# Kernel optimization log

Measured on AMD Instinct MI355X. Metric: run time of the kernel, lower is better.

The kernel has to match this reference:

```python
import jax, jax.numpy as jnp
import numpy as np

B, L, DM, H = 2, 2048, 1024, 16
D = DM // H  # head_dim = key_dim = 64


def setup_inputs() -> dict:
    key = jax.random.key(0)
    ks = jax.random.split(key, 6)
    w = 0.02
    return {
        "x": jax.random.normal(ks[0], (B, L, DM), dtype=jnp.float32),
        "wq_attn": jax.random.normal(ks[1], (DM, H * D), dtype=jnp.float32) * w,
        "wk_attn": jax.random.normal(ks[2], (DM, H * D), dtype=jnp.float32) * w,
        "wq_rel": jax.random.normal(ks[3], (DM, H * D), dtype=jnp.float32) * w,
        "wk_rel": jax.random.normal(ks[4], (DM, H * D), dtype=jnp.float32) * w,
        "wo": jax.random.normal(ks[5], (H * D, H * D), dtype=jnp.float32) * w,
    }


def reference(x, wq_attn, wk_attn, wq_rel, wk_rel, wo):
    b, l, dm = x.shape
    # projections -> (B, L, H, D); MHA so n_kv_heads == n_heads, no repeat_kv
    q = (x @ wq_attn).reshape(b, l, H, D)
    k = (x @ wk_attn).reshape(b, l, H, D)
    qr = (x @ wq_rel).reshape(b, l, H, D)
    kr = (x @ wk_rel).reshape(b, l, H, D)

    scale = D ** -0.5  # SDPA default: 1/sqrt(query key_dim)
    scores = jnp.einsum("blhd,bmhd->bhlm", q, k) * scale  # (B, H, L, L)
    causal = jnp.tril(jnp.ones((l, l), dtype=bool))
    scores = jnp.where(causal, scores, -jnp.inf)
    attn = jax.nn.softmax(scores, axis=-1)

    # attend over relational keys, then Hadamard with relational queries
    attended_kr = jnp.einsum("bhlm,bmhd->blhd", attn, kr)  # (B, L, H, D)
    attended_relations = qr * attended_kr                    # (B, L, H, D)

    out = attended_relations.reshape(b, l, H * D) @ wo       # (B, L, d_model)
    return out
```

## Files before the change

### kernel.cpp

```cpp
#include <hip/hip_runtime.h>
#include <stdint.h>


typedef __attribute__((ext_vector_type(4))) float floatx4;
typedef __attribute__((ext_vector_type(8))) short shortx8;
typedef __attribute__((ext_vector_type(4))) short shortx4;

__device__ __forceinline__ unsigned short f2bf(float f) {
    unsigned u = __float_as_uint(f);
    u += 0x7fffu + ((u >> 16) & 1u);
    return (unsigned short)(u >> 16);
}
__device__ __forceinline__ float bf2f(unsigned short s) {
    return __uint_as_float(((unsigned)s) << 16);
}
__device__ __forceinline__ float exp2fast(float x) {
#if __has_builtin(__builtin_amdgcn_exp2f)
    return __builtin_amdgcn_exp2f(x);
#else
    return __expf(x * 0.69314718056f);
#endif
}
__device__ __forceinline__ unsigned pkbf(float e0, float e1) {
    return __builtin_amdgcn_perm(__float_as_uint(e1), __float_as_uint(e0), 0x07060302u);
}
__device__ __forceinline__ floatx4 mfma16(shortx4 a, shortx4 b, floatx4 c) {
#if __has_builtin(__builtin_amdgcn_mfma_f32_16x16x16bf16_1k)
    return __builtin_amdgcn_mfma_f32_16x16x16bf16_1k(a, b, c, 0, 0, 0);
#else
    shortx8 a8 = {a[0], a[1], a[2], a[3], 0, 0, 0, 0};
    shortx8 b8 = {b[0], b[1], b[2], b[3], 0, 0, 0, 0};
    return __builtin_amdgcn_mfma_f32_16x16x32_bf16(a8, b8, c, 0, 0, 0);
#endif
}
__device__ __forceinline__ void gll16(const void* g, void* l) {
    __builtin_amdgcn_global_load_lds(
        (const __attribute__((address_space(1))) unsigned int*)g,
        (__attribute__((address_space(3))) unsigned int*)l, 16, 0, 0);
}

__global__ void k_cvt_x(const float* __restrict__ x, unsigned short* __restrict__ xb) {
    int i = (blockIdx.x * 256 + threadIdx.x) * 4;
    float4 v = *(const float4*)(x + i);
    ushort4 o;
    o.x = f2bf(v.x); o.y = f2bf(v.y); o.z = f2bf(v.z); o.w = f2bf(v.w);
    *(ushort4*)(xb + i) = o;
}

__global__ __launch_bounds__(256) void k_cvt_w5(const float* __restrict__ wq,
                                                const float* __restrict__ wk,
                                                const float* __restrict__ wqr,
                                                const float* __restrict__ wkr,
                                                const float* __restrict__ wo,
                                                unsigned short* __restrict__ wcatT,
                                                unsigned short* __restrict__ wotT) {
    __shared__ unsigned short Tl[64 * 65];
    const int t = threadIdx.x;
    const int kt = blockIdx.x * 64, nt = blockIdx.y * 64;
    const int z = blockIdx.z;
    const float* W = (z == 0) ? wq : (z == 1) ? wk : (z == 2) ? wqr : (z == 3) ? wkr : wo;
    unsigned short* outT = (z < 4) ? (wcatT + (size_t)z * 1024 * 1024) : wotT;
    const float scale = (z == 0) ? 0.18033688f : 1.0f;
    {
        const int kl = t >> 3, nc = (t & 7) * 8;
        const float* src = W + (size_t)(kt + kl) * 1024 + nt + nc;
        float a[8], b[8];
        *(float4*)(a)     = *(const float4*)(src);
        *(float4*)(a + 4) = *(const float4*)(src + 4);
        *(float4*)(b)     = *(const float4*)(src + 32 * 1024);
        *(float4*)(b + 4) = *(const float4*)(src + 32 * 1024 + 4);
#pragma unroll
        for (int i = 0; i < 8; ++i) {
            Tl[kl * 65 + nc + i]        = f2bf(a[i] * scale);
            Tl[(kl + 32) * 65 + nc + i] = f2bf(b[i] * scale);
        }
    }
    __syncthreads();
    {
        const int n = t >> 2, kc = (t & 3) * 16;
        shortx8 o0, o1;
#pragma unroll
        for (int i = 0; i < 8; ++i) {
            o0[i] = (short)Tl[(kc + i) * 65 + n];
            o1[i] = (short)Tl[(kc + 8 + i) * 65 + n];
        }
        unsigned short* dst = outT + (size_t)(nt + n) * 1024 + kt + kc;
        *(shortx8*)(dst)     = o0;
        *(shortx8*)(dst + 8) = o1;
    }
}

__global__ __launch_bounds__(256) void k_trans(const unsigned short* __restrict__ qcat,
                                               unsigned short* __restrict__ krT) {
    __shared__ unsigned short Tl[64 * 65];
    const int t = threadIdx.x;
    const int mt = blockIdx.x * 64;
    const int bh = blockIdx.y;
    const int b = bh >> 4, h = bh & 15;
    {
        const int ml = t >> 3, dc = (t & 7) * 8;
        const unsigned short* src =
            qcat + ((size_t)b * 2048 + mt + ml) * 4096 + 3072 + h * 64 + dc;
        shortx8 v0 = *(const shortx8*)(src);
        shortx8 v1 = *(const shortx8*)(src + (size_t)32 * 4096);
#pragma unroll
        for (int i = 0; i < 8; ++i) {
            Tl[ml * 65 + dc + i]        = (unsigned short)v0[i];
            Tl[(ml + 32) * 65 + dc + i] = (unsigned short)v1[i];
        }
    }
    __syncthreads();
    {
        const int d = t >> 2, mc = (t & 3) * 16;
        shortx8 o0, o1;
#pragma unroll
        for (int i = 0; i < 8; ++i) {
            o0[i] = (short)Tl[(mc + i) * 65 + d];
            o1[i] = (short)Tl[(mc + 8 + i) * 65 + d];
        }
        unsigned short* dst = krT + ((size_t)bh * 64 + d) * 2048 + mt + mc;
        *(shortx8*)(dst)     = o0;
        *(shortx8*)(dst + 8) = o1;
    }
}

__global__ __launch_bounds__(512, 1) void k_gemm_bt256(const unsigned short* __restrict__ A,
                                                       const unsigned short* __restrict__ Bt,
                                                       unsigned short* __restrict__ C,
                                                       int N, int K) {
    __shared__ alignas(16) unsigned short As[4][256 * 32];
    __shared__ alignas(16) unsigned short Bs[4][256 * 32];
    const int t = threadIdx.x;
    const int lane = t & 63, w = t >> 6;
    const int ln = lane & 15, quad = lane >> 4;
    const int wm = w >> 2, wn = w & 3;
    const int flat = blockIdx.x;
    const int xcd = flat & 7, idx = flat >> 3;
    const int bm = ((xcd >> 1) * 4 + (idx >> 3)) * 256;
    const int bn = ((xcd & 1) * 8 + (idx & 7)) * 256;

    floatx4 acc[8][4] = {};

    const int srow = t >> 2;
    const int sc = (t & 3) ^ ((srow >> 1) & 3);
    const unsigned short* gA = A + (size_t)(bm + srow) * K + sc * 8;
    const unsigned short* gB = Bt + (size_t)(bn + srow) * K + sc * 8;
    const int w16 = w * 16;

    auto stage = [&](int kt, int buf) {
        const unsigned short* a = gA + (size_t)kt * 32;
        const unsigned short* b = gB + (size_t)kt * 32;
        gll16(a,                    &As[buf][w16 * 32]);
        gll16(a + (size_t)128 * K,  &As[buf][(128 + w16) * 32]);
        gll16(b,                    &Bs[buf][w16 * 32]);
        gll16(b + (size_t)128 * K,  &Bs[buf][(128 + w16) * 32]);
    };

    const int NT = K >> 5;
    stage(0, 0); stage(1, 1); stage(2, 2);

    const int sw = (ln >> 1) & 3;
    for (int t0 = 0; t0 < NT; ++t0) {
        asm volatile("" ::: "memory");
        __builtin_amdgcn_s_barrier();
        asm volatile("" ::: "memory");
        if (t0 + 3 < NT) {
            stage(t0 + 3, (t0 + 3) & 3);
            asm volatile("s_waitcnt vmcnt(12)" ::: "memory");
        } else if (t0 + 2 < NT) {
            asm volatile("s_waitcnt vmcnt(8)" ::: "memory");
        } else if (t0 + 1 < NT) {
            asm volatile("s_waitcnt vmcnt(4)" ::: "memory");
        } else {
            asm volatile("s_waitcnt vmcnt(0)" ::: "memory");
        }
        __builtin_amdgcn_s_barrier();
        asm volatile("" ::: "memory");
        const unsigned short* Ab = As[t0 & 3];
        const unsigned short* Bb = Bs[t0 & 3];
        shortx8 bfr[4];
#pragma unroll
        for (int j = 0; j < 4; ++j)
            bfr[j] = *(const shortx8*)(Bb + (wn * 64 + j * 16 + ln) * 32 + ((quad ^ sw) * 8));
#pragma unroll
        for (int i = 0; i < 8; ++i) {
            shortx8 af = *(const shortx8*)(Ab + (wm * 128 + i * 16 + ln) * 32 + ((quad ^ sw) * 8));
#pragma unroll
            for (int j = 0; j < 4; ++j)
                acc[i][j] = __builtin_amdgcn_mfma_f32_16x16x32_bf16(af, bfr[j], acc[i][j], 0, 0, 0);
        }
    }

#pragma unroll
    for (int i = 0; i < 8; ++i)
#pragma unroll
        for (int j = 0; j < 4; ++j)
#pragma unroll
            for (int r = 0; r < 4; ++r) {
                int row = bm + wm * 128 + i * 16 + quad * 4 + r;
                int col = bn + wn * 64 + j * 16 + ln;
                C[(size_t)row * N + col] = f2bf(acc[i][j][r]);
            }
}

__global__ __launch_bounds__(256) void k_gemm_n64(const unsigned short* __restrict__ A,
                                                  const unsigned short* __restrict__ Bt,
                                                  float* __restrict__ C,
                                                  int N, int K) {
    __shared__ alignas(16) unsigned short As[4][128 * 32];
    __shared__ alignas(16) unsigned short Bs[4][64 * 32];
    const int t = threadIdx.x;
    const int lane = t & 63, wv = t >> 6;
    const int ln = lane & 15, quad = lane >> 4;
    const int bm = blockIdx.y * 128, bn = blockIdx.x * 64;

    floatx4 acc[2][4] = {};

    const int srow = t >> 2;
    const int sc = (t & 3) ^ ((srow >> 1) & 3);
    const unsigned short* gA = A + (size_t)(bm + srow) * K + sc * 8;
    const unsigned short* gB = Bt + (size_t)(bn + srow) * K + sc * 8;

    auto stage = [&](int kt, int buf) {
        const unsigned short* a = gA + (size_t)kt * 32;
        gll16(a,                   &As[buf][wv * 512]);
        gll16(a + (size_t)64 * K,  &As[buf][2048 + wv * 512]);
        gll16(gB + (size_t)kt * 32, &Bs[buf][wv * 512]);
    };

    const int NT = K >> 5;
    stage(0, 0); stage(1, 1); stage(2, 2);

    const int sw = (ln >> 1) & 3;
    for (int t0 = 0; t0 < NT; ++t0) {
        asm volatile("" ::: "memory");
        __builtin_amdgcn_s_barrier();
        asm volatile("" ::: "memory");
        if (t0 + 3 < NT) {
            stage(t0 + 3, (t0 + 3) & 3);
            asm volatile("s_waitcnt vmcnt(9)" ::: "memory");
        } else if (t0 + 2 < NT) {
            asm volatile("s_waitcnt vmcnt(6)" ::: "memory");
        } else if (t0 + 1 < NT) {
            asm volatile("s_waitcnt vmcnt(3)" ::: "memory");
        } else {
            asm volatile("s_waitcnt vmcnt(0)" ::: "memory");
        }
        __builtin_amdgcn_s_barrier();
        asm volatile("" ::: "memory");
        const unsigned short* Ab = As[t0 & 3];
        const unsigned short* Bb = Bs[t0 & 3];
        shortx8 af[2], bfr[4];
#pragma unroll
        for (int i = 0; i < 2; ++i)
            af[i] = *(const shortx8*)(Ab + (wv * 32 + i * 16 + ln) * 32 + ((quad ^ sw) * 8));
#pragma unroll
        for (int j = 0; j < 4; ++j)
            bfr[j] = *(const shortx8*)(Bb + (j * 16 + ln) * 32 + ((quad ^ sw) * 8));
#pragma unroll
        for (int i = 0; i < 2; ++i)
#pragma unroll
            for (int j = 0; j < 4; ++j)
                acc[i][j] = __builtin_amdgcn_mfma_f32_16x16x32_bf16(af[i], bfr[j], acc[i][j], 0, 0, 0);
    }

#pragma unroll
    for (int i = 0; i < 2; ++i)
#pragma unroll
        for (int j = 0; j < 4; ++j)
#pragma unroll
            for (int r = 0; r < 4; ++r) {
                int row = bm + wv * 32 + i * 16 + quad * 4 + r;
                int col = bn + j * 16 + ln;
                C[(size_t)row * N + col] = acc[i][j][r];
            }
}

__global__ __launch_bounds__(256, 2) void k_attn(const unsigned short* __restrict__ qcat,
                                                 const unsigned short* __restrict__ krT,
                                                 unsigned short* __restrict__ ar) {
    __shared__ alignas(16) unsigned short Kl[2][64 * 64];
    __shared__ alignas(16) unsigned short Rl[2][64 * 64];
    __shared__ float Ls[4][4][16];

    const int t = threadIdx.x;
    const int lane = t & 63, w = t >> 6;
    const int ln = lane & 15, quad = lane >> 4;
    const int flat = blockIdx.x;
    const int bh = (flat & 7) * 4 + ((flat >> 3) & 3);
    const int qts = flat >> 5;
    const int qt = (qts & 1) ? 31 - (qts >> 1) : (qts >> 1);
    const int b = bh >> 4, h = bh & 15;
    const int l0 = qt * 64;
    const size_t baserow = (size_t)b * 2048;

    shortx8 aq[4][2];
#pragma unroll
    for (int qc = 0; qc < 4; ++qc) {
        const unsigned short* qp =
            qcat + (baserow + l0 + qc * 16 + ln) * 4096 + h * 64 + quad * 8;
        aq[qc][0] = *(const shortx8*)(qp);
        aq[qc][1] = *(const shortx8*)(qp + 32);
    }

    floatx4 acc_o[4][4] = {};
    float lsum[4] = {0.f, 0.f, 0.f, 0.f};

    const int srow = t >> 3;
    const int sc = (t & 7) ^ (srow & 7);
    const unsigned short* gK = qcat + (baserow + srow) * 4096 + 1024 + h * 64 + sc * 8;
    const unsigned short* gR = krT + ((size_t)bh * 64 + srow) * 2048 + sc * 8;

    auto stage = [&](int kt, int buf) {
        gll16(gK + (size_t)(kt * 64) * 4096,      &Kl[buf][w * 512]);
        gll16(gK + (size_t)(kt * 64 + 32) * 4096, &Kl[buf][2048 + w * 512]);
        gll16(gR + kt * 64,                       &Rl[buf][w * 512]);
        gll16(gR + (size_t)32 * 2048 + kt * 64,   &Rl[buf][2048 + w * 512]);
    };

    stage(0, 0);
    const int swz = ln & 7;
    const int krow = (w * 16 + ln) * 64;
    const int cmw = w * 2 + (quad >> 1);
    int cur = 0;
    for (int kt = 0; kt <= qt; ++kt, cur ^= 1) {
        __syncthreads();
        if (kt < qt) stage(kt + 1, cur ^ 1);
        const unsigned short* Kc = Kl[cur];
        const unsigned short* Rc = Rl[cur];
        const bool diag = (kt == qt);

        shortx8 kf0 = *(const shortx8*)(Kc + krow + ((quad ^ swz) * 8));
        shortx8 kf1 = *(const shortx8*)(Kc + krow + (((4 + quad) ^ swz) * 8));
        shortx4 krf[4];
#pragma unroll
        for (int jd = 0; jd < 4; ++jd)
            krf[jd] = *(const shortx4*)(Rc + (jd * 16 + ln) * 64 +
                                        ((cmw ^ swz) * 8) + (quad & 1) * 4);

        const int keyb = kt * 64 + w * 16 + quad * 4;
        shortx4 pk[4];
#pragma unroll
        for (int qc = 0; qc < 4; ++qc) {
            floatx4 z = {0.f, 0.f, 0.f, 0.f};
            z = __builtin_amdgcn_mfma_f32_16x16x32_bf16(kf0, aq[qc][0], z, 0, 0, 0);
            z = __builtin_amdgcn_mfma_f32_16x16x32_bf16(kf1, aq[qc][1], z, 0, 0, 0);
            float e0 = exp2fast(z[0]);
            float e1 = exp2fast(z[1]);
            float e2 = exp2fast(z[2]);
            float e3 = exp2fast(z[3]);
            if (diag) {
                const int q = l0 + qc * 16 + ln;
                e0 = (keyb + 0 > q) ? 0.f : e0;
                e1 = (keyb + 1 > q) ? 0.f : e1;
                e2 = (keyb + 2 > q) ? 0.f : e2;
                e3 = (keyb + 3 > q) ? 0.f : e3;
            }
            lsum[qc] += (e0 + e1) + (e2 + e3);
            struct U2 { unsigned a, b; } u{pkbf(e0, e1), pkbf(e2, e3)};
            pk[qc] = __builtin_bit_cast(shortx4, u);
        }

#pragma unroll
        for (int qc = 0; qc < 4; ++qc)
#pragma unroll
            for (int jd = 0; jd < 4; ++jd)
                acc_o[qc][jd] = mfma16(krf[jd], pk[qc], acc_o[qc][jd]);
    }

#pragma unroll
    for (int qc = 0; qc < 4; ++qc) {
        float s = lsum[qc];
        s += __shfl_xor(s, 16);
        s += __shfl_xor(s, 32);
        lsum[qc] = s;
    }
    if (lane < 16) {
#pragma unroll
        for (int qc = 0; qc < 4; ++qc) Ls[w][qc][lane] = lsum[qc];
    }

    __syncthreads();
    float* redA = (float*)&Kl[0][0];
    float* redB = (float*)&Rl[0][0];
    if (w >= 2) {
        float* dst = (w == 2) ? redA : redB;
#pragma unroll
        for (int qc = 0; qc < 4; ++qc)
#pragma unroll
            for (int jd = 0; jd < 4; ++jd)
                *(floatx4*)(dst + ((qc * 4 + jd) * 64 + lane) * 4) = acc_o[qc][jd];
    }
    __syncthreads();
    if (w < 2) {
        const float* src = (w == 0) ? redA : redB;
#pragma unroll
        for (int qc = 0; qc < 4; ++qc)
#pragma unroll
            for (int jd = 0; jd < 4; ++jd)
                acc_o[qc][jd] += *(const floatx4*)(src + ((qc * 4 + jd) * 64 + lane) * 4);
    }
    __syncthreads();
    if (w == 1) {
#pragma unroll
        for (int qc = 0; qc < 4; ++qc)
#pragma unroll
            for (int jd = 0; jd < 4; ++jd)
                *(floatx4*)(redA + ((qc * 4 + jd) * 64 + lane) * 4) = acc_o[qc][jd];
    }
    __syncthreads();
    if (w == 0) {
        float inv[4];
#pragma unroll
        for (int qc = 0; qc < 4; ++qc)
            inv[qc] = 1.0f / (Ls[0][qc][ln] + Ls[1][qc][ln] + Ls[2][qc][ln] + Ls[3][qc][ln]);
#pragma unroll
        for (int qc = 0; qc < 4; ++qc) {
            const int q = l0 + qc * 16 + ln;
            const unsigned short* qr = qcat + (baserow + q) * 4096 + 2048 + h * 64;
            unsigned short* arow = ar + (baserow + q) * 1024 + h * 64;
#pragma unroll
            for (int jd = 0; jd < 4; ++jd) {
                floatx4 a = acc_o[qc][jd];
                a += *(const floatx4*)(redA + ((qc * 4 + jd) * 64 + lane) * 4);
                const int d0 = jd * 16 + quad * 4;
                shortx4 qv = *(const shortx4*)(qr + d0);
                shortx4 o;
#pragma unroll
                for (int r = 0; r < 4; ++r)
                    o[r] = (short)f2bf(a[r] * inv[qc] * bf2f((unsigned short)qv[r]));
                *(shortx4*)(arow + d0) = o;
            }
        }
    }
}

extern "C" void kernel_launch(void* const* d_in, const int* in_sizes, int n_in,
                              void* d_out, int out_size, void* d_ws, size_t ws_size,
                              hipStream_t stream) {
    const float* x   = (const float*)d_in[0];
    const float* wq  = (const float*)d_in[1];
    const float* wk  = (const float*)d_in[2];
    const float* wqr = (const float*)d_in[3];
    const float* wkr = (const float*)d_in[4];
    const float* wo  = (const float*)d_in[5];
    float* out = (float*)d_out;

    unsigned short* xb    = (unsigned short*)d_ws;
    unsigned short* wcatT = xb + (size_t)4096 * 1024;
    unsigned short* qcat  = wcatT + (size_t)4096 * 1024;
    unsigned short* wotT  = qcat + (size_t)4096 * 4096;
    unsigned short* krT   = wcatT;
    unsigned short* arb   = xb;

    k_cvt_x<<<4096, 256, 0, stream>>>(x, xb);
    k_cvt_w5<<<dim3(16, 16, 5), 256, 0, stream>>>(wq, wk, wqr, wkr, wo, wcatT, wotT);
    k_gemm_bt256<<<256, 512, 0, stream>>>(xb, wcatT, qcat, 4096, 1024);
    k_trans<<<dim3(32, 32), 256, 0, stream>>>(qcat, krT);
    k_attn<<<1024, 256, 0, stream>>>(qcat, krT, arb);
    k_gemm_n64<<<dim3(16, 32), 256, 0, stream>>>(arb, wotT, out, 1024, 1024);
}
```

Measured before the change: 201.0 us.

## Interleave LDS reads, staging and MFMA phases in GEMMs; add setprio

The large projection GEMM is restructured so each K-step runs in two half-phases. Each half reads its A/B fragments from LDS, issues the global-to-LDS prefetch for A or B separately, then runs its MFMA block at raised wave priority. The goal is to overlap LDS traffic and global staging with matrix math. The N=64 output GEMM drops from a 4-stage to a simpler 2-buffer loop, relying on __syncthreads between steps, which cuts LDS use but shortens prefetch depth. The attention PV MFMA block is also wrapped in s_setprio, and the extra barriers per step add synchronisation cost.

```diff
diff --git a/kernel.cpp b/kernel.cpp
--- a/kernel.cpp
+++ b/kernel.cpp
@@ -147,48 +147,70 @@
     const unsigned short* gB = Bt + (size_t)(bn + srow) * K + sc * 8;
     const int w16 = w * 16;
 
-    auto stage = [&](int kt, int buf) {
+    auto stageA = [&](int kt, int buf) {
         const unsigned short* a = gA + (size_t)kt * 32;
+        gll16(a,                   &As[buf][w16 * 32]);
+        gll16(a + (size_t)128 * K, &As[buf][(128 + w16) * 32]);
+    };
+    auto stageB = [&](int kt, int buf) {
         const unsigned short* b = gB + (size_t)kt * 32;
-        gll16(a,                    &As[buf][w16 * 32]);
-        gll16(a + (size_t)128 * K,  &As[buf][(128 + w16) * 32]);
-        gll16(b,                    &Bs[buf][w16 * 32]);
-        gll16(b + (size_t)128 * K,  &Bs[buf][(128 + w16) * 32]);
+        gll16(b,                   &Bs[buf][w16 * 32]);
+        gll16(b + (size_t)128 * K, &Bs[buf][(128 + w16) * 32]);
     };
 
     const int NT = K >> 5;
-    stage(0, 0); stage(1, 1); stage(2, 2);
+    stageA(0, 0); stageB(0, 0);
+    stageA(1, 1); stageB(1, 1);
+    stageA(2, 2); stageB(2, 2);
+    asm volatile("s_waitcnt vmcnt(8)" ::: "memory");
+    __builtin_amdgcn_s_barrier();
 
     const int sw = (ln >> 1) & 3;
     for (int t0 = 0; t0 < NT; ++t0) {
+        const unsigned short* Ab = As[t0 & 3];
+        const unsigned short* Bb = Bs[t0 & 3];
+        const int nb = (t0 + 3) & 3;
+        shortx8 bfr0 = *(const shortx8*)(Bb + (wn * 64 + 0 * 16 + ln) * 32 + ((quad ^ sw) * 8));
+        shortx8 bfr1 = *(const shortx8*)(Bb + (wn * 64 + 1 * 16 + ln) * 32 + ((quad ^ sw) * 8));
+        shortx8 af[8];
+#pragma unroll
+        for (int i = 0; i < 8; ++i)
+            af[i] = *(const shortx8*)(Ab + (wm * 128 + i * 16 + ln) * 32 + ((quad ^ sw) * 8));
+        if (t0 + 3 < NT) stageA(t0 + 3, nb);
         asm volatile("" ::: "memory");
         __builtin_amdgcn_s_barrier();
+        asm volatile("s_waitcnt lgkmcnt(0)" ::: "memory");
+        __builtin_amdgcn_s_setprio(1);
+#pragma unroll
+        for (int i = 0; i < 8; ++i) {
+            acc[i][0] = __builtin_amdgcn_mfma_f32_16x16x32_bf16(af[i], bfr0, acc[i][0], 0, 0, 0);
+            acc[i][1] = __builtin_amdgcn_mfma_f32_16x16x32_bf16(af[i], bfr1, acc[i][1], 0, 0, 0);
+        }
+        __builtin_amdgcn_s_setprio(0);
         asm volatile("" ::: "memory");
+        __builtin_amdgcn_s_barrier();
+        shortx8 bfr2 = *(const shortx8*)(Bb + (wn * 64 + 2 * 16 + ln) * 32 + ((quad ^ sw) * 8));
+        shortx8 bfr3 = *(const shortx8*)(Bb + (wn * 64 + 3 * 16 + ln) * 32 + ((quad ^ sw) * 8));
+        if (t0 + 3 < NT) stageB(t0 + 3, nb);
+        asm volatile("" ::: "memory");
+        __builtin_amdgcn_s_barrier();
+        asm volatile("s_waitcnt lgkmcnt(0)" ::: "memory");
+        __builtin_amdgcn_s_setprio(1);
+#pragma unroll
+        for (int i = 0; i < 8; ++i) {
+            acc[i][2] = __builtin_amdgcn_mfma_f32_16x16x32_bf16(af[i], bfr2, acc[i][2], 0, 0, 0);
+            acc[i][3] = __builtin_amdgcn_mfma_f32_16x16x32_bf16(af[i], bfr3, acc[i][3], 0, 0, 0);
+        }
+        __builtin_amdgcn_s_setprio(0);
         if (t0 + 3 < NT) {
-            stage(t0 + 3, (t0 + 3) & 3);
-            asm volatile("s_waitcnt vmcnt(12)" ::: "memory");
+            asm volatile("s_waitcnt vmcnt(8)" ::: "memory");
         } else if (t0 + 2 < NT) {
-            asm volatile("s_waitcnt vmcnt(8)" ::: "memory");
+            asm volatile("s_waitcnt vmcnt(4)" ::: "memory");
         } else if (t0 + 1 < NT) {
-            asm volatile("s_waitcnt vmcnt(4)" ::: "memory");
-        } else {
             asm volatile("s_waitcnt vmcnt(0)" ::: "memory");
         }
+        asm volatile("" ::: "memory");
         __builtin_amdgcn_s_barrier();
-        asm volatile("" ::: "memory");
-        const unsigned short* Ab = As[t0 & 3];
-        const unsigned short* Bb = Bs[t0 & 3];
-        shortx8 bfr[4];
-#pragma unroll
-        for (int j = 0; j < 4; ++j)
-            bfr[j] = *(const shortx8*)(Bb + (wn * 64 + j * 16 + ln) * 32 + ((quad ^ sw) * 8));
-#pragma unroll
-        for (int i = 0; i < 8; ++i) {
-            shortx8 af = *(const shortx8*)(Ab + (wm * 128 + i * 16 + ln) * 32 + ((quad ^ sw) * 8));
-#pragma unroll
-            for (int j = 0; j < 4; ++j)
-                acc[i][j] = __builtin_amdgcn_mfma_f32_16x16x32_bf16(af, bfr[j], acc[i][j], 0, 0, 0);
-        }
     }
 
 #pragma unroll
@@ -207,8 +229,8 @@
                                                   const unsigned short* __restrict__ Bt,
                                                   float* __restrict__ C,
                                                   int N, int K) {
-    __shared__ alignas(16) unsigned short As[4][128 * 32];
-    __shared__ alignas(16) unsigned short Bs[4][64 * 32];
+    __shared__ alignas(16) unsigned short As[2][128 * 32];
+    __shared__ alignas(16) unsigned short Bs[2][64 * 32];
     const int t = threadIdx.x;
     const int lane = t & 63, wv = t >> 6;
     const int ln = lane & 15, quad = lane >> 4;
@@ -218,45 +240,31 @@
 
     const int srow = t >> 2;
     const int sc = (t & 3) ^ ((srow >> 1) & 3);
-    const unsigned short* gA = A + (size_t)(bm + srow) * K + sc * 8;
-    const unsigned short* gB = Bt + (size_t)(bn + srow) * K + sc * 8;
-
-    auto stage = [&](int kt, int buf) {
-        const unsigned short* a = gA + (size_t)kt * 32;
-        gll16(a,                   &As[buf][wv * 512]);
-        gll16(a + (size_t)64 * K,  &As[buf][2048 + wv * 512]);
-        gll16(gB + (size_t)kt * 32, &Bs[buf][wv * 512]);
-    };
-
-    const int NT = K >> 5;
-    stage(0, 0); stage(1, 1); stage(2, 2);
+    const unsigned short* ga0 = A + (size_t)(bm + srow) * K + sc * 8;
+    const unsigned short* ga1 = ga0 + (size_t)64 * K;
+    const unsigned short* gb0 = Bt + (size_t)(bn + srow) * K + sc * 8;
+
+    gll16(ga0, &As[0][wv * 512]);
+    gll16(ga1, &As[0][2048 + wv * 512]);
+    gll16(gb0, &Bs[0][wv * 512]);
 
     const int sw = (ln >> 1) & 3;
-    for (int t0 = 0; t0 < NT; ++t0) {
-        asm volatile("" ::: "memory");
-        __builtin_amdgcn_s_barrier();
-        asm volatile("" ::: "memory");
-        if (t0 + 3 < NT) {
-            stage(t0 + 3, (t0 + 3) & 3);
-            asm volatile("s_waitcnt vmcnt(9)" ::: "memory");
-        } else if (t0 + 2 < NT) {
-            asm volatile("s_waitcnt vmcnt(6)" ::: "memory");
-        } else if (t0 + 1 < NT) {
-            asm volatile("s_waitcnt vmcnt(3)" ::: "memory");
-        } else {
-            asm volatile("s_waitcnt vmcnt(0)" ::: "memory");
-        }
-        __builtin_amdgcn_s_barrier();
-        asm volatile("" ::: "memory");
-        const unsigned short* Ab = As[t0 & 3];
-        const unsigned short* Bb = Bs[t0 & 3];
+    int cur = 0;
+    for (int k0 = 0; k0 < K; k0 += 32, cur ^= 1) {
+        __syncthreads();
+        const int nk = k0 + 32;
+        if (nk < K) {
+            gll16(ga0 + nk, &As[cur ^ 1][wv * 512]);
+            gll16(ga1 + nk, &As[cur ^ 1][2048 + wv * 512]);
+            gll16(gb0 + nk, &Bs[cur ^ 1][wv * 512]);
+        }
         shortx8 af[2], bfr[4];
 #pragma unroll
         for (int i = 0; i < 2; ++i)
-            af[i] = *(const shortx8*)(Ab + (wv * 32 + i * 16 + ln) * 32 + ((quad ^ sw) * 8));
+            af[i] = *(const shortx8*)(&As[cur][(wv * 32 + i * 16 + ln) * 32 + ((quad ^ sw) * 8)]);
 #pragma unroll
         for (int j = 0; j < 4; ++j)
-            bfr[j] = *(const shortx8*)(Bb + (j * 16 + ln) * 32 + ((quad ^ sw) * 8));
+            bfr[j] = *(const shortx8*)(&Bs[cur][(j * 16 + ln) * 32 + ((quad ^ sw) * 8)]);
 #pragma unroll
         for (int i = 0; i < 2; ++i)
 #pragma unroll
@@ -361,11 +369,13 @@
             pk[qc] = __builtin_bit_cast(shortx4, u);
         }
 
+        __builtin_amdgcn_s_setprio(1);
 #pragma unroll
         for (int qc = 0; qc < 4; ++qc)
 #pragma unroll
             for (int jd = 0; jd < 4; ++jd)
                 acc_o[qc][jd] = mfma16(krf[jd], pk[qc], acc_o[qc][jd]);
+        __builtin_amdgcn_s_setprio(0);
     }
 
 #pragma unroll
```

Result: faster. 193.3 us (-3.8%).
